# Kernel tuning notes

Hardware: AMD Instinct MI355X
Metric: run time of the kernel (lower is better)

## Reference

```python
import jax, jax.numpy as jnp
import numpy as np

B, L, D_MODEL = 2, 2048, 1024
N_HEAD, D_K, D_V = 16, 64, 64


def setup_inputs() -> dict:
    key = jax.random.key(0)
    ks = jax.random.split(key, 11)
    s = lambda fan_in: 1.0 / np.sqrt(fan_in)
    return {
        "q": jax.random.normal(ks[0], (B, L, D_MODEL), dtype=jnp.float32),
        "k": jax.random.normal(ks[1], (B, L, D_MODEL), dtype=jnp.float32),
        "v": jax.random.normal(ks[2], (B, L, D_MODEL), dtype=jnp.float32),
        "Wq": jax.random.uniform(ks[3], (D_MODEL, N_HEAD * D_K), jnp.float32, -s(D_MODEL), s(D_MODEL)),
        "bq": jax.random.uniform(ks[4], (N_HEAD * D_K,), jnp.float32, -s(D_MODEL), s(D_MODEL)),
        "Wk": jax.random.uniform(ks[5], (D_MODEL, N_HEAD * D_K), jnp.float32, -s(D_MODEL), s(D_MODEL)),
        "bk": jax.random.uniform(ks[6], (N_HEAD * D_K,), jnp.float32, -s(D_MODEL), s(D_MODEL)),
        "Wv": jax.random.uniform(ks[7], (D_MODEL, N_HEAD * D_V), jnp.float32, -s(D_MODEL), s(D_MODEL)),
        "bv": jax.random.uniform(ks[8], (N_HEAD * D_V,), jnp.float32, -s(D_MODEL), s(D_MODEL)),
        "Wo": jax.random.uniform(ks[9], (N_HEAD * D_V, D_MODEL), jnp.float32, -s(N_HEAD * D_V), s(N_HEAD * D_V)),
        "bo": jax.random.uniform(ks[10], (D_MODEL,), jnp.float32, -s(N_HEAD * D_V), s(N_HEAD * D_V)),
    }


def reference(q, k, v, Wq, bq, Wk, bk, Wv, bv, Wo, bo):
    b, lq, _ = q.shape
    lk = k.shape[1]
    # QKV projections then split heads: [B, H, L, Dk]
    qh = (q @ Wq + bq).reshape(b, lq, N_HEAD, D_K).transpose(0, 2, 1, 3)
    kh = (k @ Wk + bk).reshape(b, lk, N_HEAD, D_K).transpose(0, 2, 1, 3)
    vh = (v @ Wv + bv).reshape(b, lk, N_HEAD, D_V).transpose(0, 2, 1, 3)
    # naive SDPA: materialize [B, H, Lq, Lk] scores, scale by sqrt(d_k)
    scores = jnp.einsum("bhqd,bhkd->bhqk", qh, kh) / jnp.sqrt(jnp.float32(D_K))
    attn = jax.nn.softmax(scores, axis=-1)
    out = jnp.einsum("bhqk,bhkd->bhqd", attn, vh)
    # merge heads and output projection (dropout = identity in eval)
    out = out.transpose(0, 2, 1, 3).reshape(b, lq, N_HEAD * D_V)
    out = out @ Wo + bo
    return out, attn
```

## Files before the change

### kernel.cpp

```cpp
#include <hip/hip_runtime.h>
#include <hip/hip_bf16.h>

typedef float f32x4 __attribute__((ext_vector_type(4)));
typedef short bf16x8 __attribute__((ext_vector_type(8)));

#define MFMA_BF16 __builtin_amdgcn_mfma_f32_16x16x32_bf16

static __device__ __forceinline__ unsigned short f2bf(float f) {
    __hip_bfloat16 h = __float2bfloat16(f);
    return __builtin_bit_cast(unsigned short, h);
}
static __device__ __forceinline__ unsigned int pack2(float a, float b) {
    return (unsigned int)f2bf(a) | ((unsigned int)f2bf(b) << 16);
}

static __device__ __forceinline__ void gl16(const unsigned short* g, unsigned short* l) {
    unsigned short* gg = const_cast<unsigned short*>(g);
    __builtin_amdgcn_global_load_lds(
        (__attribute__((address_space(1))) unsigned int*)gg,
        (__attribute__((address_space(3))) unsigned int*)l, 16, 0, 0);
}

__global__ __launch_bounds__(256) void conv_wT(
    const float* __restrict__ Wq, const float* __restrict__ Wk,
    const float* __restrict__ Wv, const float* __restrict__ Wo,
    unsigned short* __restrict__ WT)
{
    const int z = blockIdx.z;
    const float* W = (z == 0) ? Wq : (z == 1) ? Wk : (z == 2) ? Wv : Wo;
    unsigned short* Wt = WT + (size_t)z * 1048576;
    const int k0 = blockIdx.x * 64, n0 = blockIdx.y * 64;
    __shared__ float tl[64][68];
    const int t = threadIdx.x;
    const int r = t >> 2, cs = (t & 3) * 16;
#pragma unroll
    for (int j = 0; j < 4; j++)
        *(float4*)&tl[r][cs + j * 4] = *(const float4*)&W[(size_t)(k0 + r) * 1024 + n0 + cs + j * 4];
    __syncthreads();
    const int n = t & 63, kb = (t >> 6) * 16;
#pragma unroll
    for (int j = 0; j < 4; j++) {
        const int kk = kb + j * 4;
        uint2 o = { pack2(tl[kk][n], tl[kk + 1][n]), pack2(tl[kk + 2][n], tl[kk + 3][n]) };
        *(uint2*)&Wt[(size_t)(n0 + n) * 1024 + k0 + kk] = o;
    }
}

__global__ __launch_bounds__(256) void conv_bf16(
    const float* __restrict__ q, const float* __restrict__ k, const float* __restrict__ v,
    unsigned short* __restrict__ qkvb)
{
    const int z = blockIdx.y;
    const float* s = (z == 0) ? q : (z == 1) ? k : v;
    unsigned short* d = qkvb + (size_t)z * 4194304;
    const size_t i = ((size_t)blockIdx.x * 256 + threadIdx.x) * 8;
    float4 a = *(const float4*)&s[i], b = *(const float4*)&s[i + 4];
    uint4 o = { pack2(a.x, a.y), pack2(a.z, a.w), pack2(b.x, b.y), pack2(b.z, b.w) };
    *(uint4*)&d[i] = o;
}

static __device__ __forceinline__ void gemm_core(
    const unsigned short* __restrict__ A, const unsigned short* __restrict__ Bt,
    unsigned short* lA, unsigned short* lB, int m0, int n0, f32x4 (&acc)[4][4])
{
    const int t = threadIdx.x;
    const int w = t >> 6, lane = t & 63, lrow = lane & 15, lkg = lane >> 4;
    const int wr = w >> 1, wc = w & 1;
    const int srow = lane >> 2, sseg = (lane & 3) * 8;

    const unsigned short* Ab0 = &A[(size_t)(m0 + w * 32 + srow) * 1024 + sseg];
    const unsigned short* Ab1 = &A[(size_t)(m0 + w * 32 + 16 + srow) * 1024 + sseg];
    const unsigned short* Bb0 = &Bt[(size_t)(n0 + w * 32 + srow) * 1024 + sseg];
    const unsigned short* Bb1 = &Bt[(size_t)(n0 + w * 32 + 16 + srow) * 1024 + sseg];

#define GISSUE(tt, buf)                                     \
    do {                                                    \
        const int k0_ = (tt) * 32;                          \
        gl16(Ab0 + k0_, &lA[(buf) * 4096 + w * 1024]);      \
        gl16(Ab1 + k0_, &lA[(buf) * 4096 + w * 1024 + 512]);\
        gl16(Bb0 + k0_, &lB[(buf) * 4096 + w * 1024]);      \
        gl16(Bb1 + k0_, &lB[(buf) * 4096 + w * 1024 + 512]);\
    } while (0)

    GISSUE(0, 0);
    GISSUE(1, 1);
    __builtin_amdgcn_sched_barrier(0);

    int bcur = 0;
    for (int tt = 0; tt < 32; ++tt) {
        if (tt < 31) { asm volatile("s_waitcnt vmcnt(4)"); }
        else         { asm volatile("s_waitcnt vmcnt(0)"); }
        __builtin_amdgcn_s_barrier();
        __builtin_amdgcn_sched_barrier(0);
        if (tt + 2 < 32) {
            int bpre = bcur + 2; if (bpre >= 3) bpre -= 3;
            GISSUE(tt + 2, bpre);
        }
        __builtin_amdgcn_sched_barrier(0);

        const unsigned short* la = &lA[bcur * 4096];
        const unsigned short* lb = &lB[bcur * 4096];
        bf16x8 af[4], bfr[4];
#pragma unroll
        for (int mi = 0; mi < 4; mi++)
            af[mi] = *(const bf16x8*)&la[(wr * 64 + mi * 16 + lrow) * 32 + lkg * 8];
#pragma unroll
        for (int ni = 0; ni < 4; ni++)
            bfr[ni] = *(const bf16x8*)&lb[(wc * 64 + ni * 16 + lrow) * 32 + lkg * 8];
        __builtin_amdgcn_s_setprio(1);
#pragma unroll
        for (int mi = 0; mi < 4; mi++)
#pragma unroll
            for (int ni = 0; ni < 4; ni++)
                acc[mi][ni] = MFMA_BF16(af[mi], bfr[ni], acc[mi][ni], 0, 0, 0);
        __builtin_amdgcn_s_setprio(0);
        bcur = (bcur == 2) ? 0 : bcur + 1;
    }
#undef GISSUE
}

__global__ __launch_bounds__(256) void gemm_qkv(
    const unsigned short* __restrict__ qkvb, const unsigned short* __restrict__ WT,
    const float* __restrict__ bq, const float* __restrict__ bk, const float* __restrict__ bv,
    unsigned short* __restrict__ Qh, unsigned short* __restrict__ Kh, unsigned short* __restrict__ Vt)
{
    const int u0 = blockIdx.x;
    const int u = (u0 & 7) * 96 + (u0 >> 3);
    const int z = u >> 8, rm = u & 255;
    const int m0 = ((rm >> 3) & 31) * 128, n0 = (rm & 7) * 128;

    const unsigned short* A = qkvb + (size_t)z * 4194304;
    const unsigned short* Bt = WT + (size_t)z * 1048576;
    const float* bias = (z == 0) ? bq : (z == 1) ? bk : bv;

    __shared__ unsigned short lA[3 * 4096], lB[3 * 4096];
    f32x4 acc[4][4];
#pragma unroll
    for (int i = 0; i < 4; i++)
#pragma unroll
        for (int j = 0; j < 4; j++) acc[i][j] = (f32x4){0.f, 0.f, 0.f, 0.f};

    gemm_core(A, Bt, lA, lB, m0, n0, acc);

    const int t = threadIdx.x;
    const int w = t >> 6, lane = t & 63, lrow = lane & 15, lkg = lane >> 4;
    const int wr = w >> 1, wc = w & 1;

#pragma unroll
    for (int mi = 0; mi < 4; mi++) {
#pragma unroll
        for (int ni = 0; ni < 4; ni++) {
            const int gn = n0 + wc * 64 + ni * 16 + lrow;
            const float bb = bias[gn];
            const int hh = gn >> 6, dk = gn & 63;
            const int gm0 = m0 + wr * 64 + mi * 16 + lkg * 4;
            const int b2 = gm0 >> 11, ll = gm0 & 2047;
            if (z < 2) {
                unsigned short* C = (z == 0) ? Qh : Kh;
#pragma unroll
                for (int r = 0; r < 4; r++)
                    C[(size_t)((b2 * 16 + hh) * 2048 + ll + r) * 64 + dk] = f2bf(acc[mi][ni][r] + bb);
            } else {
                uint2 o = { pack2(acc[mi][ni][0] + bb, acc[mi][ni][1] + bb),
                            pack2(acc[mi][ni][2] + bb, acc[mi][ni][3] + bb) };
                *(uint2*)&Vt[(size_t)((b2 * 16 + hh) * 64 + dk) * 2048 + ll] = o;
            }
        }
    }
}

__global__ __launch_bounds__(256) void gemm_o(
    const unsigned short* __restrict__ Oh, const unsigned short* __restrict__ WoT,
    const float* __restrict__ bo, float* __restrict__ out)
{
    const int u0 = blockIdx.x;
    const int u = (u0 & 7) * 32 + (u0 >> 3);
    const int m0 = (u >> 3) * 128, n0 = (u & 7) * 128;

    __shared__ unsigned short lA[3 * 4096], lB[3 * 4096];
    f32x4 acc[4][4];
#pragma unroll
    for (int i = 0; i < 4; i++)
#pragma unroll
        for (int j = 0; j < 4; j++) acc[i][j] = (f32x4){0.f, 0.f, 0.f, 0.f};

    gemm_core(Oh, WoT, lA, lB, m0, n0, acc);

    const int t = threadIdx.x;
    const int w = t >> 6, lane = t & 63, lrow = lane & 15, lkg = lane >> 4;
    const int wr = w >> 1, wc = w & 1;

#pragma unroll
    for (int mi = 0; mi < 4; mi++) {
#pragma unroll
        for (int ni = 0; ni < 4; ni++) {
            const int gn = n0 + wc * 64 + ni * 16 + lrow;
            const float bb = bo[gn];
            const int gm0 = m0 + wr * 64 + mi * 16 + lkg * 4;
#pragma unroll
            for (int r = 0; r < 4; r++)
                out[(size_t)(gm0 + r) * 1024 + gn] = acc[mi][ni][r] + bb;
        }
    }
}

__global__ __launch_bounds__(256, 4) void attn_kernel(
    const unsigned short* __restrict__ Qh, const unsigned short* __restrict__ Kh,
    const unsigned short* __restrict__ Vt, float* __restrict__ attn,
    unsigned short* __restrict__ Oh)
{
    const int bid = blockIdx.x;
    const int swz = (bid & 7) * 128 + (bid >> 3);
    const int bh = swz >> 5;
    const int q0 = (swz & 31) * 64;
    const int b = bh >> 4, h = bh & 15;
    const int t = threadIdx.x;
    const int w = t >> 6, lane = t & 63, ql = lane & 15, kg = lane >> 4;

    __shared__ unsigned short regA[8192];
    __shared__ unsigned short kv[8192];

    const size_t kvbase = (size_t)bh * 2048 * 64;
    const float C = 0.18033688011112042f;

    const unsigned short* qptr = Qh + kvbase + (size_t)(q0 + w * 16 + ql) * 64 + kg * 8;
    const bf16x8 qf0 = *(const bf16x8*)(qptr);
    const bf16x8 qf1 = *(const bf16x8*)(qptr + 32);

    const unsigned short* Kbh = Kh + kvbase;
    const unsigned short* Vbh = Vt + kvbase;

    const int kr = w * 16 + (lane >> 3);
    const int kc = (lane & 7) ^ (kr & 7);
    const int kr2 = w * 32 + (lane >> 3);
    const int kc2 = (lane & 7) ^ (kr2 & 7);
    const int r7 = ql & 7;

    f32x4 ls4 = (f32x4){0.f, 0.f, 0.f, 0.f};
    {
#pragma unroll
        for (int i = 0; i < 4; i++)
            gl16(Kbh + (size_t)(kr2 + 8 * i) * 64 + kc2 * 8, &regA[w * 2048 + i * 512]);
        __syncthreads();
        for (int kt = 0; kt < 16; ++kt) {
            unsigned short* nbuf = (kt & 1) ? regA : kv;
            if (kt < 15) {
                const int k0n = (kt + 1) * 128;
#pragma unroll
                for (int i = 0; i < 4; i++)
                    gl16(Kbh + (size_t)(k0n + kr2 + 8 * i) * 64 + kc2 * 8, &nbuf[w * 2048 + i * 512]);
            }
            const unsigned short* Kl = (kt & 1) ? kv : regA;
            f32x4 sacc[8];
            __builtin_amdgcn_s_setprio(1);
#pragma unroll
            for (int ni = 0; ni < 8; ni++) {
                const int rb = (ni * 16 + ql) * 64;
                bf16x8 kf0 = *(const bf16x8*)&Kl[rb + ((kg ^ r7) * 8)];
                bf16x8 kf1 = *(const bf16x8*)&Kl[rb + (((4 + kg) ^ r7) * 8)];
                f32x4 s = (f32x4){0.f, 0.f, 0.f, 0.f};
                s = MFMA_BF16(kf0, qf0, s, 0, 0, 0);
                sacc[ni] = MFMA_BF16(kf1, qf1, s, 0, 0, 0);
            }
            __builtin_amdgcn_s_setprio(0);
#pragma unroll
            for (int ni = 0; ni < 8; ni++)
#pragma unroll
                for (int r = 0; r < 4; r++) ls4[r] += exp2f(sacc[ni][r] * C);
            __syncthreads();
        }
        gl16(Kbh + (size_t)kr * 64 + kc * 8, &kv[w * 1024]);
        gl16(Kbh + (size_t)(kr + 8) * 64 + kc * 8, &kv[w * 1024 + 512]);
        gl16(Vbh + (size_t)kr * 2048 + kc * 8, &kv[4096 + w * 1024]);
        gl16(Vbh + (size_t)(kr + 8) * 2048 + kc * 8, &kv[4096 + w * 1024 + 512]);
    }
    float lsum = ls4[0] + ls4[1] + ls4[2] + ls4[3];
    lsum += __shfl_xor(lsum, 16);
    lsum += __shfl_xor(lsum, 32);
    const float mlg = -log2f(lsum);
    __syncthreads();

    f32x4 acco[4];
#pragma unroll
    for (int nv = 0; nv < 4; nv++) acco[nv] = (f32x4){0.f, 0.f, 0.f, 0.f};

    float* stgW = (float*)regA + w * 1024;
    const unsigned short* kvK = kv;
    const unsigned short* kvV = kv + 4096;
    float* abase = attn + ((size_t)bh * 2048 + q0 + w * 16) * 2048 + ql * 4;

    for (int kt = 0; kt < 32; ++kt) {
        const int k0 = kt * 64;

        f32x4 sacc[4];
        __builtin_amdgcn_s_setprio(1);
#pragma unroll
        for (int ni = 0; ni < 4; ni++) {
            const int rb = (ni * 16 + ql) * 64;
            bf16x8 kf0 = *(const bf16x8*)&kvK[rb + ((kg ^ r7) * 8)];
            bf16x8 kf1 = *(const bf16x8*)&kvK[rb + (((4 + kg) ^ r7) * 8)];
            f32x4 s = (f32x4){0.f, 0.f, 0.f, 0.f};
            s = MFMA_BF16(kf0, qf0, s, 0, 0, 0);
            sacc[ni] = MFMA_BF16(kf1, qf1, s, 0, 0, 0);
        }
        __builtin_amdgcn_s_setprio(0);

#pragma unroll
        for (int ni = 0; ni < 4; ni++) {
            f32x4 p;
#pragma unroll
            for (int r = 0; r < 4; r++) p[r] = exp2f(fmaf(sacc[ni][r], C, mlg));
            *(f32x4*)&stgW[ql * 64 + ni * 16 + kg * 4] = p;
        }

        __builtin_amdgcn_s_setprio(1);
#pragma unroll
        for (int s4 = 0; s4 < 2; s4++) {
            const float* ps = &stgW[ql * 64 + s4 * 32 + kg * 8];
            f32x4 pa = *(const f32x4*)ps;
            f32x4 pb = *(const f32x4*)(ps + 4);
            uint4 pw = { pack2(pa[0], pa[1]), pack2(pa[2], pa[3]),
                         pack2(pb[0], pb[1]), pack2(pb[2], pb[3]) };
            bf16x8 pf = __builtin_bit_cast(bf16x8, pw);
#pragma unroll
            for (int nv = 0; nv < 4; nv++) {
                const int cc = (s4 * 4 + kg) ^ r7;
                bf16x8 vf = *(const bf16x8*)&kvV[(nv * 16 + ql) * 64 + cc * 8];
                acco[nv] = MFMA_BF16(vf, pf, acco[nv], 0, 0, 0);
            }
        }
        __builtin_amdgcn_s_setprio(0);

        __builtin_amdgcn_s_barrier();
        __builtin_amdgcn_sched_barrier(0);

        if (kt < 31) {
            const int k0n = (kt + 1) * 64;
            gl16(Kbh + (size_t)(k0n + kr) * 64 + kc * 8, &kv[w * 1024]);
            gl16(Kbh + (size_t)(k0n + kr + 8) * 64 + kc * 8, &kv[w * 1024 + 512]);
            gl16(Vbh + (size_t)kr * 2048 + k0n + kc * 8, &kv[4096 + w * 1024]);
            gl16(Vbh + (size_t)(kr + 8) * 2048 + k0n + kc * 8, &kv[4096 + w * 1024 + 512]);
        }
        __builtin_amdgcn_sched_barrier(0);

#pragma unroll
        for (int i = 0; i < 4; i++) {
            const int row = i * 4 + kg;
            f32x4 vv = *(const f32x4*)&stgW[row * 64 + ql * 4];
            __builtin_nontemporal_store(vv, (f32x4*)&abase[(size_t)row * 2048 + k0]);
        }

        asm volatile("s_waitcnt vmcnt(4)");
        __builtin_amdgcn_s_barrier();
        __builtin_amdgcn_sched_barrier(0);
    }
    asm volatile("s_waitcnt vmcnt(0)");

    unsigned short* obase = Oh + ((size_t)(b * 2048 + q0 + w * 16 + ql)) * 1024 + h * 64 + kg * 4;
#pragma unroll
    for (int nv = 0; nv < 4; nv++) {
        uint2 o2 = { pack2(acco[nv][0], acco[nv][1]), pack2(acco[nv][2], acco[nv][3]) };
        *(uint2*)&obase[nv * 16] = o2;
    }
}

extern "C" void kernel_launch(void* const* d_in, const int* in_sizes, int n_in,
                              void* d_out, int out_size, void* d_ws, size_t ws_size,
                              hipStream_t stream) {
    const float* q  = (const float*)d_in[0];
    const float* k  = (const float*)d_in[1];
    const float* v  = (const float*)d_in[2];
    const float* Wq = (const float*)d_in[3];
    const float* bq = (const float*)d_in[4];
    const float* Wk = (const float*)d_in[5];
    const float* bk = (const float*)d_in[6];
    const float* Wv = (const float*)d_in[7];
    const float* bv = (const float*)d_in[8];
    const float* Wo = (const float*)d_in[9];
    const float* bo = (const float*)d_in[10];

    float* out  = (float*)d_out;
    float* attn = out + (size_t)2 * 2048 * 1024;

    const size_t HS = 4194304;
    unsigned short* qkvb = (unsigned short*)d_ws;
    unsigned short* WT   = qkvb + 3 * HS;
    unsigned short* Qh   = WT + 4 * 1048576;
    unsigned short* Kh   = Qh + HS;
    unsigned short* Vt   = Kh + HS;
    unsigned short* Oh   = Vt + HS;

    conv_wT  <<<dim3(16, 16, 4), 256, 0, stream>>>(Wq, Wk, Wv, Wo, WT);
    conv_bf16<<<dim3(2048, 3),  256, 0, stream>>>(q, k, v, qkvb);
    gemm_qkv <<<dim3(768), 256, 0, stream>>>(qkvb, WT, bq, bk, bv, Qh, Kh, Vt);
    attn_kernel<<<dim3(1024), 256, 0, stream>>>(Qh, Kh, Vt, attn, Oh);
    gemm_o   <<<dim3(256), 256, 0, stream>>>(Oh, WT + 3 * 1048576, bo, out);
}
```

Measured before the change: 236.8 us.

## Double-buffer K/V tiles in attention pass and merge prep kernels

The second attention pass now ping-pongs between two LDS K/V buffers. The next tile's loads are issued at the top of each iteration, so they overlap the QK, softmax, PV and attn-store work instead of sitting behind a mid-loop barrier. One barrier per iteration is dropped. LDS grows by 16 KB, so launch bounds go from 4 to 3 blocks per CU, which may reduce occupancy. Separately, the weight transpose and input bf16 conversion kernels are merged into one launch to save a kernel launch.

```diff
diff --git a/kernel.cpp b/kernel.cpp
--- a/kernel.cpp
+++ b/kernel.cpp
@@ -21,42 +21,43 @@
         (__attribute__((address_space(3))) unsigned int*)l, 16, 0, 0);
 }
 
-__global__ __launch_bounds__(256) void conv_wT(
+__global__ __launch_bounds__(256) void prep_kernel(
+    const float* __restrict__ q, const float* __restrict__ k, const float* __restrict__ v,
     const float* __restrict__ Wq, const float* __restrict__ Wk,
     const float* __restrict__ Wv, const float* __restrict__ Wo,
-    unsigned short* __restrict__ WT)
+    unsigned short* __restrict__ WT, unsigned short* __restrict__ qkvb)
 {
-    const int z = blockIdx.z;
-    const float* W = (z == 0) ? Wq : (z == 1) ? Wk : (z == 2) ? Wv : Wo;
-    unsigned short* Wt = WT + (size_t)z * 1048576;
-    const int k0 = blockIdx.x * 64, n0 = blockIdx.y * 64;
-    __shared__ float tl[64][68];
+    const int bid = blockIdx.x;
     const int t = threadIdx.x;
-    const int r = t >> 2, cs = (t & 3) * 16;
-#pragma unroll
-    for (int j = 0; j < 4; j++)
-        *(float4*)&tl[r][cs + j * 4] = *(const float4*)&W[(size_t)(k0 + r) * 1024 + n0 + cs + j * 4];
-    __syncthreads();
-    const int n = t & 63, kb = (t >> 6) * 16;
-#pragma unroll
-    for (int j = 0; j < 4; j++) {
-        const int kk = kb + j * 4;
-        uint2 o = { pack2(tl[kk][n], tl[kk + 1][n]), pack2(tl[kk + 2][n], tl[kk + 3][n]) };
-        *(uint2*)&Wt[(size_t)(n0 + n) * 1024 + k0 + kk] = o;
-    }
-}
-
-__global__ __launch_bounds__(256) void conv_bf16(
-    const float* __restrict__ q, const float* __restrict__ k, const float* __restrict__ v,
-    unsigned short* __restrict__ qkvb)
-{
-    const int z = blockIdx.y;
-    const float* s = (z == 0) ? q : (z == 1) ? k : v;
-    unsigned short* d = qkvb + (size_t)z * 4194304;
-    const size_t i = ((size_t)blockIdx.x * 256 + threadIdx.x) * 8;
-    float4 a = *(const float4*)&s[i], b = *(const float4*)&s[i + 4];
-    uint4 o = { pack2(a.x, a.y), pack2(a.z, a.w), pack2(b.x, b.y), pack2(b.z, b.w) };
-    *(uint4*)&d[i] = o;
+    if (bid < 1024) {
+        const int z = bid >> 8, rem = bid & 255;
+        const int k0 = (rem & 15) * 64, n0 = (rem >> 4) * 64;
+        const float* W = (z == 0) ? Wq : (z == 1) ? Wk : (z == 2) ? Wv : Wo;
+        unsigned short* Wt = WT + (size_t)z * 1048576;
+        __shared__ float tl[64][68];
+        const int r = t >> 2, cs = (t & 3) * 16;
+#pragma unroll
+        for (int j = 0; j < 4; j++)
+            *(float4*)&tl[r][cs + j * 4] = *(const float4*)&W[(size_t)(k0 + r) * 1024 + n0 + cs + j * 4];
+        __syncthreads();
+        const int n = t & 63, kb = (t >> 6) * 16;
+#pragma unroll
+        for (int j = 0; j < 4; j++) {
+            const int kk = kb + j * 4;
+            uint2 o = { pack2(tl[kk][n], tl[kk + 1][n]), pack2(tl[kk + 2][n], tl[kk + 3][n]) };
+            *(uint2*)&Wt[(size_t)(n0 + n) * 1024 + k0 + kk] = o;
+        }
+    } else {
+        const int idx = bid - 1024;
+        const int z = idx >> 11;
+        const int xb = idx & 2047;
+        const float* s = (z == 0) ? q : (z == 1) ? k : v;
+        unsigned short* d = qkvb + (size_t)z * 4194304;
+        const size_t i = ((size_t)xb * 256 + t) * 8;
+        float4 a = *(const float4*)&s[i], b = *(const float4*)&s[i + 4];
+        uint4 o = { pack2(a.x, a.y), pack2(a.z, a.w), pack2(b.x, b.y), pack2(b.z, b.w) };
+        *(uint4*)&d[i] = o;
+    }
 }
 
 static __device__ __forceinline__ void gemm_core(
@@ -204,7 +205,7 @@
     }
 }
 
-__global__ __launch_bounds__(256, 4) void attn_kernel(
+__global__ __launch_bounds__(256, 3) void attn_kernel(
     const unsigned short* __restrict__ Qh, const unsigned short* __restrict__ Kh,
     const unsigned short* __restrict__ Vt, float* __restrict__ attn,
     unsigned short* __restrict__ Oh)
@@ -218,7 +219,7 @@
     const int w = t >> 6, lane = t & 63, ql = lane & 15, kg = lane >> 4;
 
     __shared__ unsigned short regA[8192];
-    __shared__ unsigned short kv[8192];
+    __shared__ unsigned short kv[16384];
 
     const size_t kvbase = (size_t)bh * 2048 * 64;
     const float C = 0.18033688011112042f;
@@ -236,6 +237,9 @@
     const int kc2 = (lane & 7) ^ (kr2 & 7);
     const int r7 = ql & 7;
 
+    unsigned short* kv0 = &kv[0];
+    unsigned short* kv1 = &kv[8192];
+
     f32x4 ls4 = (f32x4){0.f, 0.f, 0.f, 0.f};
     {
 #pragma unroll
@@ -243,14 +247,14 @@
             gl16(Kbh + (size_t)(kr2 + 8 * i) * 64 + kc2 * 8, &regA[w * 2048 + i * 512]);
         __syncthreads();
         for (int kt = 0; kt < 16; ++kt) {
-            unsigned short* nbuf = (kt & 1) ? regA : kv;
+            unsigned short* nbuf = (kt & 1) ? regA : kv0;
             if (kt < 15) {
                 const int k0n = (kt + 1) * 128;
 #pragma unroll
                 for (int i = 0; i < 4; i++)
                     gl16(Kbh + (size_t)(k0n + kr2 + 8 * i) * 64 + kc2 * 8, &nbuf[w * 2048 + i * 512]);
             }
-            const unsigned short* Kl = (kt & 1) ? kv : regA;
+            const unsigned short* Kl = (kt & 1) ? kv0 : regA;
             f32x4 sacc[8];
             __builtin_amdgcn_s_setprio(1);
 #pragma unroll
@@ -269,28 +273,44 @@
                 for (int r = 0; r < 4; r++) ls4[r] += exp2f(sacc[ni][r] * C);
             __syncthreads();
         }
-        gl16(Kbh + (size_t)kr * 64 + kc * 8, &kv[w * 1024]);
-        gl16(Kbh + (size_t)(kr + 8) * 64 + kc * 8, &kv[w * 1024 + 512]);
-        gl16(Vbh + (size_t)kr * 2048 + kc * 8, &kv[4096 + w * 1024]);
-        gl16(Vbh + (size_t)(kr + 8) * 2048 + kc * 8, &kv[4096 + w * 1024 + 512]);
+        gl16(Kbh + (size_t)kr * 64 + kc * 8, &kv0[w * 1024]);
+        gl16(Kbh + (size_t)(kr + 8) * 64 + kc * 8, &kv0[w * 1024 + 512]);
+        gl16(Vbh + (size_t)kr * 2048 + kc * 8, &kv0[4096 + w * 1024]);
+        gl16(Vbh + (size_t)(kr + 8) * 2048 + kc * 8, &kv0[4096 + w * 1024 + 512]);
+        __builtin_amdgcn_sched_barrier(0);
     }
     float lsum = ls4[0] + ls4[1] + ls4[2] + ls4[3];
     lsum += __shfl_xor(lsum, 16);
     lsum += __shfl_xor(lsum, 32);
     const float mlg = -log2f(lsum);
-    __syncthreads();
 
     f32x4 acco[4];
 #pragma unroll
     for (int nv = 0; nv < 4; nv++) acco[nv] = (f32x4){0.f, 0.f, 0.f, 0.f};
 
     float* stgW = (float*)regA + w * 1024;
-    const unsigned short* kvK = kv;
-    const unsigned short* kvV = kv + 4096;
     float* abase = attn + ((size_t)bh * 2048 + q0 + w * 16) * 2048 + ql * 4;
 
     for (int kt = 0; kt < 32; ++kt) {
         const int k0 = kt * 64;
+        if (kt == 0) { asm volatile("s_waitcnt vmcnt(0)"); }
+        else         { asm volatile("s_waitcnt vmcnt(4)"); }
+        __builtin_amdgcn_s_barrier();
+        __builtin_amdgcn_sched_barrier(0);
+
+        unsigned short* cur = (kt & 1) ? kv1 : kv0;
+        if (kt < 31) {
+            unsigned short* nxt = (kt & 1) ? kv0 : kv1;
+            const int k0n = (kt + 1) * 64;
+            gl16(Kbh + (size_t)(k0n + kr) * 64 + kc * 8, &nxt[w * 1024]);
+            gl16(Kbh + (size_t)(k0n + kr + 8) * 64 + kc * 8, &nxt[w * 1024 + 512]);
+            gl16(Vbh + (size_t)kr * 2048 + k0n + kc * 8, &nxt[4096 + w * 1024]);
+            gl16(Vbh + (size_t)(kr + 8) * 2048 + k0n + kc * 8, &nxt[4096 + w * 1024 + 512]);
+        }
+        __builtin_amdgcn_sched_barrier(0);
+
+        const unsigned short* kvK = cur;
+        const unsigned short* kvV = cur + 4096;
 
         f32x4 sacc[4];
         __builtin_amdgcn_s_setprio(1);
@@ -331,28 +351,12 @@
         }
         __builtin_amdgcn_s_setprio(0);
 
-        __builtin_amdgcn_s_barrier();
-        __builtin_amdgcn_sched_barrier(0);
-
-        if (kt < 31) {
-            const int k0n = (kt + 1) * 64;
-            gl16(Kbh + (size_t)(k0n + kr) * 64 + kc * 8, &kv[w * 1024]);
-            gl16(Kbh + (size_t)(k0n + kr + 8) * 64 + kc * 8, &kv[w * 1024 + 512]);
-            gl16(Vbh + (size_t)kr * 2048 + k0n + kc * 8, &kv[4096 + w * 1024]);
-            gl16(Vbh + (size_t)(kr + 8) * 2048 + k0n + kc * 8, &kv[4096 + w * 1024 + 512]);
-        }
-        __builtin_amdgcn_sched_barrier(0);
-
 #pragma unroll
         for (int i = 0; i < 4; i++) {
             const int row = i * 4 + kg;
             f32x4 vv = *(const f32x4*)&stgW[row * 64 + ql * 4];
             __builtin_nontemporal_store(vv, (f32x4*)&abase[(size_t)row * 2048 + k0]);
         }
-
-        asm volatile("s_waitcnt vmcnt(4)");
-        __builtin_amdgcn_s_barrier();
-        __builtin_amdgcn_sched_barrier(0);
     }
     asm volatile("s_waitcnt vmcnt(0)");
 
@@ -390,9 +394,8 @@
     unsigned short* Vt   = Kh + HS;
     unsigned short* Oh   = Vt + HS;
 
-    conv_wT  <<<dim3(16, 16, 4), 256, 0, stream>>>(Wq, Wk, Wv, Wo, WT);
-    conv_bf16<<<dim3(2048, 3),  256, 0, stream>>>(q, k, v, qkvb);
-    gemm_qkv <<<dim3(768), 256, 0, stream>>>(qkvb, WT, bq, bk, bv, Qh, Kh, Vt);
+    prep_kernel<<<dim3(7168), 256, 0, stream>>>(q, k, v, Wq, Wk, Wv, Wo, WT, qkvb);
+    gemm_qkv   <<<dim3(768),  256, 0, stream>>>(qkvb, WT, bq, bk, bv, Qh, Kh, Vt);
     attn_kernel<<<dim3(1024), 256, 0, stream>>>(Qh, Kh, Vt, attn, Oh);
-    gemm_o   <<<dim3(256), 256, 0, stream>>>(Oh, WT + 3 * 1048576, bo, out);
-}
+    gemm_o     <<<dim3(256),  256, 0, stream>>>(Oh, WT + 3 * 1048576, bo, out);
+}
```

Measured after the change: 242.5 us. +2.4%, slower.
